# Kernel tuning notes

Measured on AMD Instinct MI355X. Metric: run time of the kernel, lower is better.

## Reference

```python
import jax, jax.numpy as jnp
import numpy as np

B, L, E = 128, 512, 128
NUM_Q, NUM_C, DIFF = 10000, 300, 100


def _lin(k, fan_in, fan_out):
    kw, kb = jax.random.split(k)
    s = 1.0 / np.sqrt(fan_in)
    W = jax.random.uniform(kw, (fan_in, fan_out), jnp.float32, -s, s)
    b = jax.random.uniform(kb, (fan_out,), jnp.float32, -s, s)
    return W, b


def setup_inputs() -> dict:
    key = jax.random.key(0)
    ks = jax.random.split(key, 24)
    inp = {
        "q": jax.random.randint(ks[0], (B, L), 0, NUM_Q),
        "c": jax.random.randint(ks[1], (B, L), 0, NUM_C),
        "sd": jax.random.randint(ks[2], (B, L), 0, DIFF + 99),
        "qd": jax.random.randint(ks[3], (B, L), 0, DIFF + 99),
        "a": jax.random.randint(ks[4], (B, L), 0, 2 * NUM_Q + 1),
        "qshft": jax.random.randint(ks[5], (B, L), 0, NUM_Q),
        "cshft": jax.random.randint(ks[6], (B, L), 0, NUM_C),
        "sdshft": jax.random.randint(ks[7], (B, L), 0, DIFF + 99),
        "qdshft": jax.random.randint(ks[8], (B, L), 0, DIFF + 99),
        "knowledge": jax.random.normal(ks[9], (1, E), jnp.float32) * 0.1,
        "q_tab": jax.random.normal(ks[10], (NUM_Q + 1, E), jnp.float32),
        "c_tab": jax.random.normal(ks[11], (NUM_C + 1, E), jnp.float32),
        "sd_tab": jax.random.normal(ks[12], (DIFF + 100, E), jnp.float32),
        "qd_tab": jax.random.normal(ks[13], (DIFF + 100, E), jnp.float32),
        "a_tab": jax.random.normal(ks[14], (2 * NUM_Q + 2, E), jnp.float32),
    }
    for name, fan_in, ki in [("1", 4 * E, 15), ("2", E, 16), ("3", E, 17),
                             ("4", 2 * E, 18), ("5", 2 * E, 19), ("6", 4 * E, 20)]:
        W, b = _lin(ks[ki], fan_in, E)
        inp[f"W{name}"], inp[f"b{name}"] = W, b
    Wf, bf = _lin(ks[21], E, 10)
    inp["Wf"], inp["bf"] = Wf, bf
    return inp


def reference(q, c, sd, qd, a, qshft, cshft, sdshft, qdshft,
              knowledge, q_tab, c_tab, sd_tab, qd_tab, a_tab,
              W1, b1, W2, b2, W3, b3, W4, b4, W5, b5, W6, b6, Wf, bf):
    # Embedding lookups  [B, L, E]
    q_e, c_e = q_tab[q], c_tab[c]
    sd_e, qd_e = sd_tab[sd], qd_tab[qd]
    a_e = a_tab[a]
    # input_data = linear_1(cat(q,c,sd,qd))  [B, L, E]
    inp = jnp.concatenate([q_e, c_e, sd_e, qd_e], -1) @ W1 + b1
    # (target_data in the torch code is dead: never used for the output)

    k0 = jnp.broadcast_to(knowledge, (q.shape[0], knowledge.shape[1]))  # [B, E]

    def step(k, xs):
        x, sd1, a1, qd1 = xs  # each [B, E]
        qq = x - k
        SDFt = jax.nn.sigmoid(qq @ W2 + b2) * jnp.tanh(qq @ W3 + b3)  # dropout=eval
        xa = jnp.concatenate([SDFt, a1], -1)
        PKAt = jax.nn.sigmoid(xa @ W4 + b4) * jnp.tanh(xa @ W5 + b5)
        ins = jnp.concatenate([k, a1, sd1, qd1], -1)
        gK = jax.nn.sigmoid(ins @ W6 + b6)
        k_new = gK * k + (1.0 - gK) * PKAt
        return k_new, k_new @ Wf + bf

    xs = (jnp.swapaxes(inp, 0, 1), jnp.swapaxes(sd_e, 0, 1),
          jnp.swapaxes(a_e, 0, 1), jnp.swapaxes(qd_e, 0, 1))  # [L, B, E]
    _, logits = jax.lax.scan(step, k0, xs)  # [L, B, 10]
    return jax.nn.sigmoid(jnp.swapaxes(logits, 0, 1))  # [B, L, 10]
```

## Files before the change

kernel.cpp:

```cpp
#include <hip/hip_runtime.h>
#include <hip/hip_bf16.h>
#include <stdint.h>

#define E_DIM 128
#define L_SEQ 512
#define B_SZ  128

typedef _Float16 h2 __attribute__((ext_vector_type(2)));
typedef _Float16 f16x8 __attribute__((ext_vector_type(8)));
typedef float f32x4 __attribute__((ext_vector_type(4)));

constexpr size_t SZ_W12 = 512 * 128 * 4;
constexpr size_t SZ_TQ  = 10001 * 128 * 4;
constexpr size_t SZ_TC  = 301 * 128 * 4;
constexpr size_t SZ_TS  = 200 * 128 * 4;
constexpr size_t SZ_TA  = 20002 * 128 * 4;

constexpr size_t OFF_W12  = 0;
constexpr size_t OFF_W13  = OFF_W12 + SZ_W12;
constexpr size_t OFF_BV2  = OFF_W13 + SZ_W12;
constexpr size_t OFF_BV3  = OFF_BV2 + 512;
constexpr size_t OFF_TQ2  = OFF_BV3 + 512;
constexpr size_t OFF_TQ3  = OFF_TQ2 + SZ_TQ;
constexpr size_t OFF_TC2  = OFF_TQ3 + SZ_TQ;
constexpr size_t OFF_TC3  = OFF_TC2 + SZ_TC;
constexpr size_t OFF_TSD2 = OFF_TC3 + SZ_TC;
constexpr size_t OFF_TSD3 = OFF_TSD2 + SZ_TS;
constexpr size_t OFF_TSD6 = OFF_TSD3 + SZ_TS;
constexpr size_t OFF_TQD2 = OFF_TSD6 + SZ_TS;
constexpr size_t OFF_TQD3 = OFF_TQD2 + SZ_TS;
constexpr size_t OFF_TQD6 = OFF_TQD3 + SZ_TS;
constexpr size_t OFF_TA4  = OFF_TQD6 + SZ_TS;
constexpr size_t OFF_TA5  = OFF_TA4 + SZ_TA;
constexpr size_t OFF_TA6  = OFF_TA5 + SZ_TA;
constexpr size_t OFF_K    = OFF_TA6 + SZ_TA;

__device__ __forceinline__ float fdot2f(unsigned int a, unsigned int b, float c) {
#if __has_builtin(__builtin_amdgcn_fdot2)
  return __builtin_amdgcn_fdot2(__builtin_bit_cast(h2, a), __builtin_bit_cast(h2, b), c, false);
#else
  h2 x = __builtin_bit_cast(h2, a), y = __builtin_bit_cast(h2, b);
  return c + (float)x[0] * (float)y[0] + (float)x[1] * (float)y[1];
#endif
}

__device__ __forceinline__ unsigned int packh2(float a, float b) {
  h2 v; v[0] = (_Float16)a; v[1] = (_Float16)b;
  return __builtin_bit_cast(unsigned int, v);
}

__device__ __forceinline__ float fsig(float x) {
  float t = __builtin_amdgcn_exp2f(-1.4426950408889634f * x);
  return __builtin_amdgcn_rcpf(1.0f + t);
}
__device__ __forceinline__ float ftanh(float x) {
  float t = __builtin_amdgcn_exp2f(2.8853900817779268f * x);
  return 1.0f - 2.0f * __builtin_amdgcn_rcpf(t + 1.0f);
}

#define BARRIER_RAW() asm volatile("s_waitcnt lgkmcnt(0)\n\ts_barrier" ::: "memory")

__global__ __launch_bounds__(128, 1) void prepA_kernel(
    const float* __restrict__ W1, const float* __restrict__ W2, const float* __restrict__ W3,
    const float* __restrict__ b1, const float* __restrict__ b2, const float* __restrict__ b3,
    char* __restrict__ ws) {
  float* W12 = (float*)(ws + OFF_W12);
  float* W13 = (float*)(ws + OFF_W13);
  float* bv2 = (float*)(ws + OFF_BV2);
  float* bv3 = (float*)(ws + OFF_BV3);
  __shared__ __align__(16) float rowb[8][128];
  const int j = threadIdx.x;
  const int blk = blockIdx.x;
  if (blk < 8) {
    const float* M = (blk < 4) ? W2 : W3;
    float* dst = (blk < 4) ? W12 : W13;
    const int r0 = (blk & 3) * 128;
    float Mcol[128];
#pragma unroll
    for (int t = 0; t < 128; t++) Mcol[t] = M[t * 128 + j];
    for (int rb = 0; rb < 128; rb += 8) {
#pragma unroll
      for (int rr = 0; rr < 8; rr++) rowb[rr][j] = W1[(r0 + rb + rr) * 128 + j];
      __syncthreads();
#pragma unroll
      for (int rr = 0; rr < 8; rr++) {
        float acc = 0.0f;
        const float4* r4 = (const float4*)rowb[rr];
#pragma unroll
        for (int t4 = 0; t4 < 32; t4++) {
          float4 v = r4[t4];
          acc += v.x * Mcol[4 * t4 + 0];
          acc += v.y * Mcol[4 * t4 + 1];
          acc += v.z * Mcol[4 * t4 + 2];
          acc += v.w * Mcol[4 * t4 + 3];
        }
        dst[(r0 + rb + rr) * 128 + j] = acc;
      }
      __syncthreads();
    }
  } else {
    rowb[0][j] = b1[j];
    __syncthreads();
    float a2 = b2[j], a3 = b3[j];
    for (int t = 0; t < 128; t++) {
      float bb = rowb[0][t];
      a2 += bb * W2[t * 128 + j];
      a3 += bb * W3[t * 128 + j];
    }
    bv2[j] = a2;
    bv3[j] = a3;
  }
}

template <int NSEG>
__global__ __launch_bounds__(256, 1) void gemm_tabs_kernel(
    const float* __restrict__ q_tab, const float* __restrict__ c_tab,
    const float* __restrict__ sd_tab, const float* __restrict__ qd_tab,
    const float* __restrict__ a_tab,
    const float* __restrict__ W4, const float* __restrict__ W5, const float* __restrict__ W6,
    const float* __restrict__ b4, const float* __restrict__ b5, const float* __restrict__ b6,
    char* __restrict__ ws) {
  constexpr int WD  = NSEG * 128;
  constexpr int SPAN = WD / 4;
  constexpr int NCT = SPAN / 16;

  __shared__ _Float16 BT[WD][136];
  __shared__ _Float16 At[32][136];
  __shared__ float biasL[384];

  const float* W12 = (const float*)(ws + OFF_W12);
  const float* W13 = (const float*)(ws + OFF_W13);
  const float* bv2 = (const float*)(ws + OFF_BV2);
  const float* bv3 = (const float*)(ws + OFF_BV3);

  const int bid = blockIdx.x;
  const int tid = threadIdx.x;
  const int wv = tid >> 6, ln = tid & 63;

  const float* src; int rows; int blk_in;
  const float* bsrc[3]; int koff[3]; const float* bias[3]; float* dst[3];
  if (NSEG == 2) {
    if (bid < 79) { src = q_tab; rows = 10001; blk_in = bid;
      bsrc[0] = W12; bsrc[1] = W13; koff[0] = koff[1] = 0;
      bias[0] = bv2; bias[1] = bv3;
      dst[0] = (float*)(ws + OFF_TQ2); dst[1] = (float*)(ws + OFF_TQ3);
    } else { src = c_tab; rows = 301; blk_in = bid - 79;
      bsrc[0] = W12; bsrc[1] = W13; koff[0] = koff[1] = 128;
      bias[0] = bias[1] = nullptr;
      dst[0] = (float*)(ws + OFF_TC2); dst[1] = (float*)(ws + OFF_TC3);
    }
    bsrc[2] = nullptr; koff[2] = 0; bias[2] = nullptr; dst[2] = nullptr;
  } else {
    if (bid < 2) { src = sd_tab; rows = 200; blk_in = bid;
      bsrc[0] = W12; bsrc[1] = W13; bsrc[2] = W6; koff[0] = koff[1] = koff[2] = 256;
      bias[0] = bias[1] = bias[2] = nullptr;
      dst[0] = (float*)(ws + OFF_TSD2); dst[1] = (float*)(ws + OFF_TSD3); dst[2] = (float*)(ws + OFF_TSD6);
    } else if (bid < 4) { src = qd_tab; rows = 200; blk_in = bid - 2;
      bsrc[0] = W12; bsrc[1] = W13; bsrc[2] = W6; koff[0] = koff[1] = koff[2] = 384;
      bias[0] = bias[1] = bias[2] = nullptr;
      dst[0] = (float*)(ws + OFF_TQD2); dst[1] = (float*)(ws + OFF_TQD3); dst[2] = (float*)(ws + OFF_TQD6);
    } else { src = a_tab; rows = 20002; blk_in = bid - 4;
      bsrc[0] = W4; bsrc[1] = W5; bsrc[2] = W6; koff[0] = koff[1] = koff[2] = 128;
      bias[0] = b4; bias[1] = b5; bias[2] = b6;
      dst[0] = (float*)(ws + OFF_TA4); dst[1] = (float*)(ws + OFF_TA5); dst[2] = (float*)(ws + OFF_TA6);
    }
  }

#pragma unroll
  for (int s = 0; s < NSEG; s++) {
    const float* M = bsrc[s] + (size_t)koff[s] * 128;
    const int jj = tid & 127, kb = tid >> 7;
    for (int k0 = 0; k0 < 128; k0 += 2) {
      const int k = k0 + kb;
      BT[s * 128 + jj][k] = (_Float16)M[k * 128 + jj];
    }
    if (tid < 128) biasL[s * 128 + tid] = bias[s] ? bias[s][tid] : 0.0f;
  }
  __syncthreads();

  f16x8 bf[NCT][4];
#pragma unroll
  for (int ct = 0; ct < NCT; ct++)
#pragma unroll
    for (int kt = 0; kt < 4; kt++) {
      const int col = wv * SPAN + ct * 16 + (ln & 15);
      const int k = kt * 32 + (ln >> 4) * 8;
      bf[ct][kt] = *(const f16x8*)&BT[col][k];
    }
  float bvl[NCT];
#pragma unroll
  for (int ct = 0; ct < NCT; ct++) bvl[ct] = biasL[wv * SPAN + ct * 16 + (ln & 15)];

  const int row_base = blk_in * 128;
  for (int ch = 0; ch < 4; ch++) {
    const int row0 = row_base + ch * 32;
    {
      const int r = tid >> 3, cb = (tid & 7) * 16;
      int sr = row0 + r; if (sr >= rows) sr = rows - 1;
      const float4* s4 = (const float4*)(src + (size_t)sr * 128 + cb);
      float4 v0 = s4[0], v1 = s4[1], v2 = s4[2], v3 = s4[3];
      f16x8 lo, hi;
      lo[0] = (_Float16)v0.x; lo[1] = (_Float16)v0.y; lo[2] = (_Float16)v0.z; lo[3] = (_Float16)v0.w;
      lo[4] = (_Float16)v1.x; lo[5] = (_Float16)v1.y; lo[6] = (_Float16)v1.z; lo[7] = (_Float16)v1.w;
      hi[0] = (_Float16)v2.x; hi[1] = (_Float16)v2.y; hi[2] = (_Float16)v2.z; hi[3] = (_Float16)v2.w;
      hi[4] = (_Float16)v3.x; hi[5] = (_Float16)v3.y; hi[6] = (_Float16)v3.z; hi[7] = (_Float16)v3.w;
      *(f16x8*)&At[r][cb] = lo;
      *(f16x8*)&At[r][cb + 8] = hi;
    }
    __syncthreads();
    f16x8 af[2][4];
#pragma unroll
    for (int rt = 0; rt < 2; rt++)
#pragma unroll
      for (int kt = 0; kt < 4; kt++) {
        const int row = rt * 16 + (ln & 15);
        const int k = kt * 32 + (ln >> 4) * 8;
        af[rt][kt] = *(const f16x8*)&At[row][k];
      }
    f32x4 acc[2][NCT];
#pragma unroll
    for (int rt = 0; rt < 2; rt++)
#pragma unroll
      for (int ct = 0; ct < NCT; ct++) acc[rt][ct] = (f32x4){0.f, 0.f, 0.f, 0.f};
#pragma unroll
    for (int kt = 0; kt < 4; kt++)
#pragma unroll
      for (int ct = 0; ct < NCT; ct++)
#pragma unroll
        for (int rt = 0; rt < 2; rt++)
          acc[rt][ct] = __builtin_amdgcn_mfma_f32_16x16x32_f16(af[rt][kt], bf[ct][kt], acc[rt][ct], 0, 0, 0);
#pragma unroll
    for (int ct = 0; ct < NCT; ct++) {
      const int gcol = wv * SPAN + ct * 16 + (ln & 15);
      const int seg = gcol >> 7, col = gcol & 127;
      float* D = dst[seg];
      const float bv = bvl[ct];
#pragma unroll
      for (int rt = 0; rt < 2; rt++)
#pragma unroll
        for (int e = 0; e < 4; e++) {
          const int row = row0 + rt * 16 + (ln >> 4) * 4 + e;
          if (row < rows) D[(size_t)row * 128 + col] = acc[rt][ct][e] + bv;
        }
    }
    __syncthreads();
  }
}


#define PREFETCH(S, P) do {                                                   \
    int _s = (S);                                                             \
    int _qi = idxb[0][_s], _ci = idxb[1][_s], _si = idxb[2][_s];              \
    int _di = idxb[3][_s], _ai = idxb[4][_s];                                 \
    P##q2 = Tq2[_qi * 128 + j]; P##q3 = Tq3[_qi * 128 + j];                   \
    P##c2 = Tc2[_ci * 128 + j]; P##c3 = Tc3[_ci * 128 + j];                   \
    P##s2 = Ts2[_si * 128 + j]; P##s3 = Ts3[_si * 128 + j];                   \
    P##s6 = Ts6[_si * 128 + j];                                               \
    P##d2 = Td2[_di * 128 + j]; P##d3 = Td3[_di * 128 + j];                   \
    P##d6 = Td6[_di * 128 + j];                                               \
    P##a4 = Ta4[_ai * 128 + j]; P##a5 = Ta5[_ai * 128 + j];                   \
    P##a6 = Ta6[_ai * 128 + j];                                               \
  } while (0)

#define SCAN_STEP(P, S2, L) do {                                              \
    float u2a = 0.f, u2b = 0.f, u3a = 0.f, u3b = 0.f, u6a = 0.f, u6b = 0.f;   \
    {                                                                         \
      const uint4* kp4 = ((const uint4*)kpair) + 8 * h;                       \
      _Pragma("unroll")                                                       \
      for (int i = 0; i < 8; i++) {                                           \
        uint4 kv = kp4[i];                                                    \
        u2a = fdot2f(kv.x, w2h[4 * i + 0], u2a);                              \
        u3a = fdot2f(kv.x, w3h[4 * i + 0], u3a);                              \
        u6a = fdot2f(kv.x, w6h[4 * i + 0], u6a);                              \
        u2b = fdot2f(kv.y, w2h[4 * i + 1], u2b);                              \
        u3b = fdot2f(kv.y, w3h[4 * i + 1], u3b);                              \
        u6b = fdot2f(kv.y, w6h[4 * i + 1], u6b);                              \
        u2a = fdot2f(kv.z, w2h[4 * i + 2], u2a);                              \
        u3a = fdot2f(kv.z, w3h[4 * i + 2], u3a);                              \
        u6a = fdot2f(kv.z, w6h[4 * i + 2], u6a);                              \
        u2b = fdot2f(kv.w, w2h[4 * i + 3], u2b);                              \
        u3b = fdot2f(kv.w, w3h[4 * i + 3], u3b);                              \
        u6b = fdot2f(kv.w, w6h[4 * i + 3], u6b);                              \
      }                                                                       \
    }                                                                         \
    float U2p = u2a + u2b, U3p = u3a + u3b, U6p = u6a + u6b;                  \
    U2p += __shfl_xor(U2p, 32);                                               \
    U3p += __shfl_xor(U3p, 32);                                               \
    U6p += __shfl_xor(U6p, 32);                                               \
    float U2 = (P##q2 + P##c2 + P##s2 + P##d2) - U2p;                         \
    float U3 = (P##q3 + P##c3 + P##s3 + P##d3) - U3p;                         \
    float U6 = (P##a6 + P##s6 + P##d6) + U6p;                                 \
    float sdft = fsig(U2) * ftanh(U3);                                        \
    float g = fsig(U6);                                                       \
    if (!h) ((_Float16*)sdfp)[j] = (_Float16)sdft;                            \
    BARRIER_RAW();                                    \
    float u4a = 0.f, u4b = 0.f, u5a = 0.f, u5b = 0.f;                         \
    {                                                                         \
      const uint4* sp4 = ((const uint4*)sdfp) + 8 * h;                        \
      _Pragma("unroll")                                                       \
      for (int i = 0; i < 8; i++) {                                           \
        uint4 sv = sp4[i];                                                    \
        u4a = fdot2f(sv.x, w4h[4 * i + 0], u4a);                              \
        u5a = fdot2f(sv.x, w5h[4 * i + 0], u5a);                              \
        u4b = fdot2f(sv.y, w4h[4 * i + 1], u4b);                              \
        u5b = fdot2f(sv.y, w5h[4 * i + 1], u5b);                              \
        u4a = fdot2f(sv.z, w4h[4 * i + 2], u4a);                              \
        u5a = fdot2f(sv.z, w5h[4 * i + 2], u5a);                              \
        u4b = fdot2f(sv.w, w4h[4 * i + 3], u4b);                              \
        u5b = fdot2f(sv.w, w5h[4 * i + 3], u5b);                              \
      }                                                                       \
    }                                                                         \
    float U4p = u4a + u4b, U5p = u5a + u5b;                                   \
    U4p += __shfl_xor(U4p, 32);                                               \
    U5p += __shfl_xor(U5p, 32);                                               \
    float pk = fsig(U4p + P##a4) * ftanh(U5p + P##a5);                        \
    k = g * k + (1.0f - g) * pk;                                              \
    if (h) ((_Float16*)kpair)[j] = (_Float16)k;                               \
    if (!h) Kout[((size_t)(base + (L))) * 128 + j] = k;                       \
    PREFETCH(S2, P);                                                          \
    BARRIER_RAW();                                       \
  } while (0)

__global__ __launch_bounds__(256, 1) void scan_kernel(
    const int* __restrict__ q, const int* __restrict__ c, const int* __restrict__ sd,
    const int* __restrict__ qd, const int* __restrict__ a,
    const float* __restrict__ knowledge,
    const float* __restrict__ W2, const float* __restrict__ W3, const float* __restrict__ W4,
    const float* __restrict__ W5, const float* __restrict__ W6,
    char* __restrict__ ws) {
  const int tid = threadIdx.x;
  const int wv = tid >> 6, ln = tid & 63;
  const int j = (wv << 5) | (ln & 31);
  const int h = ln >> 5;
  const int b = blockIdx.x;
  const int base = b * L_SEQ;

  const float* Tq2 = (const float*)(ws + OFF_TQ2);
  const float* Tq3 = (const float*)(ws + OFF_TQ3);
  const float* Tc2 = (const float*)(ws + OFF_TC2);
  const float* Tc3 = (const float*)(ws + OFF_TC3);
  const float* Ts2 = (const float*)(ws + OFF_TSD2);
  const float* Ts3 = (const float*)(ws + OFF_TSD3);
  const float* Ts6 = (const float*)(ws + OFF_TSD6);
  const float* Td2 = (const float*)(ws + OFF_TQD2);
  const float* Td3 = (const float*)(ws + OFF_TQD3);
  const float* Td6 = (const float*)(ws + OFF_TQD6);
  const float* Ta4 = (const float*)(ws + OFF_TA4);
  const float* Ta5 = (const float*)(ws + OFF_TA5);
  const float* Ta6 = (const float*)(ws + OFF_TA6);
  float* Kout = (float*)(ws + OFF_K);

  __shared__ int idxb[5][L_SEQ];
  __shared__ __align__(16) unsigned int kpair[64];
  __shared__ __align__(16) unsigned int sdfp[64];

  idxb[0][tid] = q[base + tid];  idxb[0][tid + 256] = q[base + tid + 256];
  idxb[1][tid] = c[base + tid];  idxb[1][tid + 256] = c[base + tid + 256];
  idxb[2][tid] = sd[base + tid]; idxb[2][tid + 256] = sd[base + tid + 256];
  idxb[3][tid] = qd[base + tid]; idxb[3][tid + 256] = qd[base + tid + 256];
  idxb[4][tid] = a[base + tid];  idxb[4][tid + 256] = a[base + tid + 256];

  unsigned int w2h[32], w3h[32], w6h[32], w4h[32], w5h[32];
  const int t0 = h * 64;
#pragma unroll
  for (int p = 0; p < 32; p++) {
    w2h[p] = packh2(W2[(t0 + 2 * p) * 128 + j], W2[(t0 + 2 * p + 1) * 128 + j]);
    w3h[p] = packh2(W3[(t0 + 2 * p) * 128 + j], W3[(t0 + 2 * p + 1) * 128 + j]);
    w6h[p] = packh2(W6[(t0 + 2 * p) * 128 + j], W6[(t0 + 2 * p + 1) * 128 + j]);
    w4h[p] = packh2(W4[(t0 + 2 * p) * 128 + j], W4[(t0 + 2 * p + 1) * 128 + j]);
    w5h[p] = packh2(W5[(t0 + 2 * p) * 128 + j], W5[(t0 + 2 * p + 1) * 128 + j]);
  }

  float k = knowledge[j];
  if (h) ((_Float16*)kpair)[j] = (_Float16)k;
  __syncthreads();

  float gAq2, gAq3, gAc2, gAc3, gAs2, gAs3, gAs6, gAd2, gAd3, gAd6, gAa4, gAa5, gAa6;
  float gBq2, gBq3, gBc2, gBc3, gBs2, gBs3, gBs6, gBd2, gBd3, gBd6, gBa4, gBa5, gBa6;
  PREFETCH(0, gA);
  PREFETCH(1, gB);

#pragma unroll 1
  for (int m = 0; m < L_SEQ / 2; m++) {
    const int l0 = 2 * m;
    const int s2 = (l0 + 2 < L_SEQ) ? (l0 + 2) : (L_SEQ - 1);
    const int s3 = (l0 + 3 < L_SEQ) ? (l0 + 3) : (L_SEQ - 1);
    SCAN_STEP(gA, s2, l0);
    SCAN_STEP(gB, s3, l0 + 1);
  }
}

__global__ __launch_bounds__(256, 2) void logits_kernel(
    const float* __restrict__ Wf, const float* __restrict__ bf,
    const char* __restrict__ ws, float* __restrict__ out) {
  __shared__ float WfL[1280];
  __shared__ float bfL[10];
  const int tid = threadIdx.x;
  for (int i = tid; i < 1280; i += 256) WfL[i] = Wf[i];
  if (tid < 10) bfL[tid] = bf[tid];
  __syncthreads();
  const float* K = (const float*)(ws + OFF_K);
  const int nrows = B_SZ * L_SEQ;
  for (int r = blockIdx.x * 256 + tid; r < nrows; r += gridDim.x * 256) {
    const float4* kr = (const float4*)(K + (size_t)r * 128);
    float acc[10];
#pragma unroll
    for (int i = 0; i < 10; i++) acc[i] = bfL[i];
#pragma unroll
    for (int t4 = 0; t4 < 32; t4++) {
      float4 v = kr[t4];
#pragma unroll
      for (int i = 0; i < 10; i++)
        acc[i] += v.x * WfL[(4 * t4 + 0) * 10 + i] + v.y * WfL[(4 * t4 + 1) * 10 + i] +
                  v.z * WfL[(4 * t4 + 2) * 10 + i] + v.w * WfL[(4 * t4 + 3) * 10 + i];
    }
    float* o = out + (size_t)r * 10;
#pragma unroll
    for (int i = 0; i < 10; i++) o[i] = fsig(acc[i]);
  }
}

extern "C" void kernel_launch(void* const* d_in, const int* in_sizes, int n_in,
                              void* d_out, int out_size, void* d_ws, size_t ws_size,
                              hipStream_t stream) {
  const int* q  = (const int*)d_in[0];
  const int* c  = (const int*)d_in[1];
  const int* sd = (const int*)d_in[2];
  const int* qd = (const int*)d_in[3];
  const int* a  = (const int*)d_in[4];
  const float* knowledge = (const float*)d_in[9];
  const float* q_tab  = (const float*)d_in[10];
  const float* c_tab  = (const float*)d_in[11];
  const float* sd_tab = (const float*)d_in[12];
  const float* qd_tab = (const float*)d_in[13];
  const float* a_tab  = (const float*)d_in[14];
  const float* W1 = (const float*)d_in[15];
  const float* b1 = (const float*)d_in[16];
  const float* W2 = (const float*)d_in[17];
  const float* b2 = (const float*)d_in[18];
  const float* W3 = (const float*)d_in[19];
  const float* b3 = (const float*)d_in[20];
  const float* W4 = (const float*)d_in[21];
  const float* b4 = (const float*)d_in[22];
  const float* W5 = (const float*)d_in[23];
  const float* b5 = (const float*)d_in[24];
  const float* W6 = (const float*)d_in[25];
  const float* b6 = (const float*)d_in[26];
  const float* Wf = (const float*)d_in[27];
  const float* bf = (const float*)d_in[28];
  char* ws = (char*)d_ws;
  float* out = (float*)d_out;

  prepA_kernel<<<9, 128, 0, stream>>>(W1, W2, W3, b1, b2, b3, ws);
  gemm_tabs_kernel<2><<<82, 256, 0, stream>>>(q_tab, c_tab, sd_tab, qd_tab, a_tab,
                                              W4, W5, W6, b4, b5, b6, ws);
  gemm_tabs_kernel<3><<<161, 256, 0, stream>>>(q_tab, c_tab, sd_tab, qd_tab, a_tab,
                                               W4, W5, W6, b4, b5, b6, ws);
  scan_kernel<<<B_SZ, 256, 0, stream>>>(q, c, sd, qd, a, knowledge, W2, W3, W4, W5, W6, ws);
  logits_kernel<<<256, 256, 0, stream>>>(Wf, bf, ws, out);
}
```

Before: 793.8 us.

## Repartition precompute kernels across more blocks and pack two sequences per scan block

The W1·W2/W1·W3 fold is spread over 513 small blocks instead of 9, and the two table-GEMM launches become one launch with 647 blocks, one output matrix each. This is meant to raise GPU occupancy in the preparation phase. The scan kernel now runs two independent batch sequences per 512-thread block, each with its own index and shared exchange buffers. That halves the scan grid to 64 blocks but lets the two sequences' barrier-bound latency overlap on a CU, at the cost of block-wide barriers coupling the two groups.

After: 883.6 us. 1.11x slower.

```diff
diff --git a/kernel.cpp b/kernel.cpp
--- a/kernel.cpp
+++ b/kernel.cpp
@@ -60,7 +60,7 @@
 
 #define BARRIER_RAW() asm volatile("s_waitcnt lgkmcnt(0)\n\ts_barrier" ::: "memory")
 
-__global__ __launch_bounds__(128, 1) void prepA_kernel(
+__global__ __launch_bounds__(256, 2) void prepA_kernel(
     const float* __restrict__ W1, const float* __restrict__ W2, const float* __restrict__ W3,
     const float* __restrict__ b1, const float* __restrict__ b2, const float* __restrict__ b3,
     char* __restrict__ ws) {
@@ -68,130 +68,110 @@
   float* W13 = (float*)(ws + OFF_W13);
   float* bv2 = (float*)(ws + OFF_BV2);
   float* bv3 = (float*)(ws + OFF_BV3);
-  __shared__ __align__(16) float rowb[8][128];
-  const int j = threadIdx.x;
-  const int blk = blockIdx.x;
-  if (blk < 8) {
-    const float* M = (blk < 4) ? W2 : W3;
-    float* dst = (blk < 4) ? W12 : W13;
-    const int r0 = (blk & 3) * 128;
-    float Mcol[128];
-#pragma unroll
-    for (int t = 0; t < 128; t++) Mcol[t] = M[t * 128 + j];
-    for (int rb = 0; rb < 128; rb += 8) {
-#pragma unroll
-      for (int rr = 0; rr < 8; rr++) rowb[rr][j] = W1[(r0 + rb + rr) * 128 + j];
-      __syncthreads();
-#pragma unroll
-      for (int rr = 0; rr < 8; rr++) {
-        float acc = 0.0f;
-        const float4* r4 = (const float4*)rowb[rr];
-#pragma unroll
-        for (int t4 = 0; t4 < 32; t4++) {
-          float4 v = r4[t4];
-          acc += v.x * Mcol[4 * t4 + 0];
-          acc += v.y * Mcol[4 * t4 + 1];
-          acc += v.z * Mcol[4 * t4 + 2];
-          acc += v.w * Mcol[4 * t4 + 3];
-        }
-        dst[(r0 + rb + rr) * 128 + j] = acc;
-      }
-      __syncthreads();
+  const int blk = blockIdx.x, tid = threadIdx.x;
+  if (blk < 512) {
+    const int m = blk >> 8;
+    const int rp = blk & 255;
+    const float* M = m ? W3 : W2;
+    float* dst = m ? W13 : W12;
+    const int rr = tid >> 7, j = tid & 127;
+    const int r = rp * 2 + rr;
+    __shared__ float rowL[2][128];
+    rowL[rr][j] = W1[r * 128 + j];
+    __syncthreads();
+    float acc = 0.0f;
+#pragma unroll 8
+    for (int t = 0; t < 128; t++) acc += rowL[rr][t] * M[t * 128 + j];
+    dst[r * 128 + j] = acc;
+  } else if (tid < 128) {
+    float a2 = b2[tid], a3 = b3[tid];
+    for (int t = 0; t < 128; t++) {
+      float bb = b1[t];
+      a2 += bb * W2[t * 128 + tid];
+      a3 += bb * W3[t * 128 + tid];
     }
-  } else {
-    rowb[0][j] = b1[j];
-    __syncthreads();
-    float a2 = b2[j], a3 = b3[j];
-    for (int t = 0; t < 128; t++) {
-      float bb = rowb[0][t];
-      a2 += bb * W2[t * 128 + j];
-      a3 += bb * W3[t * 128 + j];
-    }
-    bv2[j] = a2;
-    bv3[j] = a3;
-  }
-}
-
-template <int NSEG>
-__global__ __launch_bounds__(256, 1) void gemm_tabs_kernel(
+    bv2[tid] = a2;
+    bv3[tid] = a3;
+  }
+}
+
+__global__ __launch_bounds__(256, 2) void gemm_tab1_kernel(
     const float* __restrict__ q_tab, const float* __restrict__ c_tab,
     const float* __restrict__ sd_tab, const float* __restrict__ qd_tab,
     const float* __restrict__ a_tab,
     const float* __restrict__ W4, const float* __restrict__ W5, const float* __restrict__ W6,
     const float* __restrict__ b4, const float* __restrict__ b5, const float* __restrict__ b6,
     char* __restrict__ ws) {
-  constexpr int WD  = NSEG * 128;
-  constexpr int SPAN = WD / 4;
-  constexpr int NCT = SPAN / 16;
-
-  __shared__ _Float16 BT[WD][136];
+  __shared__ _Float16 BT[128][136];
   __shared__ _Float16 At[32][136];
-  __shared__ float biasL[384];
+  __shared__ float biasL[128];
 
   const float* W12 = (const float*)(ws + OFF_W12);
   const float* W13 = (const float*)(ws + OFF_W13);
-  const float* bv2 = (const float*)(ws + OFF_BV2);
-  const float* bv3 = (const float*)(ws + OFF_BV3);
-
-  const int bid = blockIdx.x;
-  const int tid = threadIdx.x;
+  const float* bv2f = (const float*)(ws + OFF_BV2);
+  const float* bv3f = (const float*)(ws + OFF_BV3);
+
+  const int bid = blockIdx.x, tid = threadIdx.x;
   const int wv = tid >> 6, ln = tid & 63;
 
-  const float* src; int rows; int blk_in;
-  const float* bsrc[3]; int koff[3]; const float* bias[3]; float* dst[3];
-  if (NSEG == 2) {
-    if (bid < 79) { src = q_tab; rows = 10001; blk_in = bid;
-      bsrc[0] = W12; bsrc[1] = W13; koff[0] = koff[1] = 0;
-      bias[0] = bv2; bias[1] = bv3;
-      dst[0] = (float*)(ws + OFF_TQ2); dst[1] = (float*)(ws + OFF_TQ3);
-    } else { src = c_tab; rows = 301; blk_in = bid - 79;
-      bsrc[0] = W12; bsrc[1] = W13; koff[0] = koff[1] = 128;
-      bias[0] = bias[1] = nullptr;
-      dst[0] = (float*)(ws + OFF_TC2); dst[1] = (float*)(ws + OFF_TC3);
+  int task, rb;
+  if      (bid < 79)  { task = 0;  rb = bid; }
+  else if (bid < 158) { task = 1;  rb = bid - 79; }
+  else if (bid < 161) { task = 2;  rb = bid - 158; }
+  else if (bid < 164) { task = 3;  rb = bid - 161; }
+  else if (bid < 166) { task = 4;  rb = bid - 164; }
+  else if (bid < 168) { task = 5;  rb = bid - 166; }
+  else if (bid < 170) { task = 6;  rb = bid - 168; }
+  else if (bid < 172) { task = 7;  rb = bid - 170; }
+  else if (bid < 174) { task = 8;  rb = bid - 172; }
+  else if (bid < 176) { task = 9;  rb = bid - 174; }
+  else if (bid < 333) { task = 10; rb = bid - 176; }
+  else if (bid < 490) { task = 11; rb = bid - 333; }
+  else                { task = 12; rb = bid - 490; }
+
+  const float* src; int rows; const float* Bsrc; const float* bias; float* dst;
+  switch (task) {
+    case 0:  src = q_tab;  rows = 10001; Bsrc = W12;            bias = bv2f;   dst = (float*)(ws + OFF_TQ2);  break;
+    case 1:  src = q_tab;  rows = 10001; Bsrc = W13;            bias = bv3f;   dst = (float*)(ws + OFF_TQ3);  break;
+    case 2:  src = c_tab;  rows = 301;   Bsrc = W12 + 128*128;  bias = nullptr; dst = (float*)(ws + OFF_TC2);  break;
+    case 3:  src = c_tab;  rows = 301;   Bsrc = W13 + 128*128;  bias = nullptr; dst = (float*)(ws + OFF_TC3);  break;
+    case 4:  src = sd_tab; rows = 200;   Bsrc = W12 + 256*128;  bias = nullptr; dst = (float*)(ws + OFF_TSD2); break;
+    case 5:  src = sd_tab; rows = 200;   Bsrc = W13 + 256*128;  bias = nullptr; dst = (float*)(ws + OFF_TSD3); break;
+    case 6:  src = sd_tab; rows = 200;   Bsrc = W6  + 256*128;  bias = nullptr; dst = (float*)(ws + OFF_TSD6); break;
+    case 7:  src = qd_tab; rows = 200;   Bsrc = W12 + 384*128;  bias = nullptr; dst = (float*)(ws + OFF_TQD2); break;
+    case 8:  src = qd_tab; rows = 200;   Bsrc = W13 + 384*128;  bias = nullptr; dst = (float*)(ws + OFF_TQD3); break;
+    case 9:  src = qd_tab; rows = 200;   Bsrc = W6  + 384*128;  bias = nullptr; dst = (float*)(ws + OFF_TQD6); break;
+    case 10: src = a_tab;  rows = 20002; Bsrc = W4  + 128*128;  bias = b4;     dst = (float*)(ws + OFF_TA4);  break;
+    case 11: src = a_tab;  rows = 20002; Bsrc = W5  + 128*128;  bias = b5;     dst = (float*)(ws + OFF_TA5);  break;
+    default: src = a_tab;  rows = 20002; Bsrc = W6  + 128*128;  bias = b6;     dst = (float*)(ws + OFF_TA6);  break;
+  }
+
+#pragma unroll
+  for (int r = 0; r < 8; r++) {
+    const int k = (tid >> 4) + r * 16;
+    const int j0 = (tid & 15) * 8;
+    float4 v0 = *(const float4*)(Bsrc + k * 128 + j0);
+    float4 v1 = *(const float4*)(Bsrc + k * 128 + j0 + 4);
+    BT[j0 + 0][k] = (_Float16)v0.x; BT[j0 + 1][k] = (_Float16)v0.y;
+    BT[j0 + 2][k] = (_Float16)v0.z; BT[j0 + 3][k] = (_Float16)v0.w;
+    BT[j0 + 4][k] = (_Float16)v1.x; BT[j0 + 5][k] = (_Float16)v1.y;
+    BT[j0 + 6][k] = (_Float16)v1.z; BT[j0 + 7][k] = (_Float16)v1.w;
+  }
+  if (tid < 128) biasL[tid] = bias ? bias[tid] : 0.0f;
+  __syncthreads();
+
+  f16x8 bfr[2][4];
+#pragma unroll
+  for (int ct = 0; ct < 2; ct++)
+#pragma unroll
+    for (int kt = 0; kt < 4; kt++) {
+      const int col = wv * 32 + ct * 16 + (ln & 15);
+      const int k = kt * 32 + (ln >> 4) * 8;
+      bfr[ct][kt] = *(const f16x8*)&BT[col][k];
     }
-    bsrc[2] = nullptr; koff[2] = 0; bias[2] = nullptr; dst[2] = nullptr;
-  } else {
-    if (bid < 2) { src = sd_tab; rows = 200; blk_in = bid;
-      bsrc[0] = W12; bsrc[1] = W13; bsrc[2] = W6; koff[0] = koff[1] = koff[2] = 256;
-      bias[0] = bias[1] = bias[2] = nullptr;
-      dst[0] = (float*)(ws + OFF_TSD2); dst[1] = (float*)(ws + OFF_TSD3); dst[2] = (float*)(ws + OFF_TSD6);
-    } else if (bid < 4) { src = qd_tab; rows = 200; blk_in = bid - 2;
-      bsrc[0] = W12; bsrc[1] = W13; bsrc[2] = W6; koff[0] = koff[1] = koff[2] = 384;
-      bias[0] = bias[1] = bias[2] = nullptr;
-      dst[0] = (float*)(ws + OFF_TQD2); dst[1] = (float*)(ws + OFF_TQD3); dst[2] = (float*)(ws + OFF_TQD6);
-    } else { src = a_tab; rows = 20002; blk_in = bid - 4;
-      bsrc[0] = W4; bsrc[1] = W5; bsrc[2] = W6; koff[0] = koff[1] = koff[2] = 128;
-      bias[0] = b4; bias[1] = b5; bias[2] = b6;
-      dst[0] = (float*)(ws + OFF_TA4); dst[1] = (float*)(ws + OFF_TA5); dst[2] = (float*)(ws + OFF_TA6);
-    }
-  }
-
-#pragma unroll
-  for (int s = 0; s < NSEG; s++) {
-    const float* M = bsrc[s] + (size_t)koff[s] * 128;
-    const int jj = tid & 127, kb = tid >> 7;
-    for (int k0 = 0; k0 < 128; k0 += 2) {
-      const int k = k0 + kb;
-      BT[s * 128 + jj][k] = (_Float16)M[k * 128 + jj];
-    }
-    if (tid < 128) biasL[s * 128 + tid] = bias[s] ? bias[s][tid] : 0.0f;
-  }
-  __syncthreads();
-
-  f16x8 bf[NCT][4];
-#pragma unroll
-  for (int ct = 0; ct < NCT; ct++)
-#pragma unroll
-    for (int kt = 0; kt < 4; kt++) {
-      const int col = wv * SPAN + ct * 16 + (ln & 15);
-      const int k = kt * 32 + (ln >> 4) * 8;
-      bf[ct][kt] = *(const f16x8*)&BT[col][k];
-    }
-  float bvl[NCT];
-#pragma unroll
-  for (int ct = 0; ct < NCT; ct++) bvl[ct] = biasL[wv * SPAN + ct * 16 + (ln & 15)];
-
-  const int row_base = blk_in * 128;
+  float bvl[2] = { biasL[wv * 32 + (ln & 15)], biasL[wv * 32 + 16 + (ln & 15)] };
+
+  const int row_base = rb * 128;
   for (int ch = 0; ch < 4; ch++) {
     const int row0 = row_base + ch * 32;
     {
@@ -217,30 +197,28 @@
         const int k = kt * 32 + (ln >> 4) * 8;
         af[rt][kt] = *(const f16x8*)&At[row][k];
       }
-    f32x4 acc[2][NCT];
+    f32x4 acc[2][2];
 #pragma unroll
     for (int rt = 0; rt < 2; rt++)
 #pragma unroll
-      for (int ct = 0; ct < NCT; ct++) acc[rt][ct] = (f32x4){0.f, 0.f, 0.f, 0.f};
+      for (int ct = 0; ct < 2; ct++) acc[rt][ct] = (f32x4){0.f, 0.f, 0.f, 0.f};
 #pragma unroll
     for (int kt = 0; kt < 4; kt++)
 #pragma unroll
-      for (int ct = 0; ct < NCT; ct++)
+      for (int ct = 0; ct < 2; ct++)
 #pragma unroll
         for (int rt = 0; rt < 2; rt++)
-          acc[rt][ct] = __builtin_amdgcn_mfma_f32_16x16x32_f16(af[rt][kt], bf[ct][kt], acc[rt][ct], 0, 0, 0);
-#pragma unroll
-    for (int ct = 0; ct < NCT; ct++) {
-      const int gcol = wv * SPAN + ct * 16 + (ln & 15);
-      const int seg = gcol >> 7, col = gcol & 127;
-      float* D = dst[seg];
+          acc[rt][ct] = __builtin_amdgcn_mfma_f32_16x16x32_f16(af[rt][kt], bfr[ct][kt], acc[rt][ct], 0, 0, 0);
+#pragma unroll
+    for (int ct = 0; ct < 2; ct++) {
+      const int col = wv * 32 + ct * 16 + (ln & 15);
       const float bv = bvl[ct];
 #pragma unroll
       for (int rt = 0; rt < 2; rt++)
 #pragma unroll
         for (int e = 0; e < 4; e++) {
           const int row = row0 + rt * 16 + (ln >> 4) * 4 + e;
-          if (row < rows) D[(size_t)row * 128 + col] = acc[rt][ct][e] + bv;
+          if (row < rows) dst[(size_t)row * 128 + col] = acc[rt][ct][e] + bv;
         }
     }
     __syncthreads();
@@ -250,8 +228,8 @@
 
 #define PREFETCH(S, P) do {                                                   \
     int _s = (S);                                                             \
-    int _qi = idxb[0][_s], _ci = idxb[1][_s], _si = idxb[2][_s];              \
-    int _di = idxb[3][_s], _ai = idxb[4][_s];                                 \
+    int _qi = idxb[g][0][_s], _ci = idxb[g][1][_s], _si = idxb[g][2][_s];     \
+    int _di = idxb[g][3][_s], _ai = idxb[g][4][_s];                           \
     P##q2 = Tq2[_qi * 128 + j]; P##q3 = Tq3[_qi * 128 + j];                   \
     P##c2 = Tc2[_ci * 128 + j]; P##c3 = Tc3[_ci * 128 + j];                   \
     P##s2 = Ts2[_si * 128 + j]; P##s3 = Ts3[_si * 128 + j];                   \
@@ -265,7 +243,7 @@
 #define SCAN_STEP(P, S2, L) do {                                              \
     float u2a = 0.f, u2b = 0.f, u3a = 0.f, u3b = 0.f, u6a = 0.f, u6b = 0.f;   \
     {                                                                         \
-      const uint4* kp4 = ((const uint4*)kpair) + 8 * h;                       \
+      const uint4* kp4 = ((const uint4*)kpair[g]) + 8 * h;                    \
       _Pragma("unroll")                                                       \
       for (int i = 0; i < 8; i++) {                                           \
         uint4 kv = kp4[i];                                                    \
@@ -291,12 +269,12 @@
     float U3 = (P##q3 + P##c3 + P##s3 + P##d3) - U3p;                         \
     float U6 = (P##a6 + P##s6 + P##d6) + U6p;                                 \
     float sdft = fsig(U2) * ftanh(U3);                                        \
-    float g = fsig(U6);                                                       \
-    if (!h) ((_Float16*)sdfp)[j] = (_Float16)sdft;                            \
+    float g_ = fsig(U6);                                                      \
+    if (!h) ((_Float16*)sdfp[g])[j] = (_Float16)sdft;                         \
     BARRIER_RAW();                                    \
     float u4a = 0.f, u4b = 0.f, u5a = 0.f, u5b = 0.f;                         \
     {                                                                         \
-      const uint4* sp4 = ((const uint4*)sdfp) + 8 * h;                        \
+      const uint4* sp4 = ((const uint4*)sdfp[g]) + 8 * h;                     \
       _Pragma("unroll")                                                       \
       for (int i = 0; i < 8; i++) {                                           \
         uint4 sv = sp4[i];                                                    \
@@ -314,14 +292,14 @@
     U4p += __shfl_xor(U4p, 32);                                               \
     U5p += __shfl_xor(U5p, 32);                                               \
     float pk = fsig(U4p + P##a4) * ftanh(U5p + P##a5);                        \
-    k = g * k + (1.0f - g) * pk;                                              \
-    if (h) ((_Float16*)kpair)[j] = (_Float16)k;                               \
+    k = g_ * k + (1.0f - g_) * pk;                                            \
+    if (h) ((_Float16*)kpair[g])[j] = (_Float16)k;                            \
     if (!h) Kout[((size_t)(base + (L))) * 128 + j] = k;                       \
     PREFETCH(S2, P);                                                          \
     BARRIER_RAW();                                       \
   } while (0)
 
-__global__ __launch_bounds__(256, 1) void scan_kernel(
+__global__ __launch_bounds__(512, 2) void scan_kernel(
     const int* __restrict__ q, const int* __restrict__ c, const int* __restrict__ sd,
     const int* __restrict__ qd, const int* __restrict__ a,
     const float* __restrict__ knowledge,
@@ -329,10 +307,13 @@
     const float* __restrict__ W5, const float* __restrict__ W6,
     char* __restrict__ ws) {
   const int tid = threadIdx.x;
-  const int wv = tid >> 6, ln = tid & 63;
-  const int j = (wv << 5) | (ln & 31);
+  const int g = tid >> 8;
+  const int t256 = tid & 255;
+  const int ln = tid & 63;
+  const int wvl = (t256 >> 6);
+  const int j = (wvl << 5) | (ln & 31);
   const int h = ln >> 5;
-  const int b = blockIdx.x;
+  const int b = (blockIdx.x << 1) | g;
   const int base = b * L_SEQ;
 
   const float* Tq2 = (const float*)(ws + OFF_TQ2);
@@ -350,15 +331,15 @@
   const float* Ta6 = (const float*)(ws + OFF_TA6);
   float* Kout = (float*)(ws + OFF_K);
 
-  __shared__ int idxb[5][L_SEQ];
-  __shared__ __align__(16) unsigned int kpair[64];
-  __shared__ __align__(16) unsigned int sdfp[64];
-
-  idxb[0][tid] = q[base + tid];  idxb[0][tid + 256] = q[base + tid + 256];
-  idxb[1][tid] = c[base + tid];  idxb[1][tid + 256] = c[base + tid + 256];
-  idxb[2][tid] = sd[base + tid]; idxb[2][tid + 256] = sd[base + tid + 256];
-  idxb[3][tid] = qd[base + tid]; idxb[3][tid + 256] = qd[base + tid + 256];
-  idxb[4][tid] = a[base + tid];  idxb[4][tid + 256] = a[base + tid + 256];
+  __shared__ int idxb[2][5][L_SEQ];
+  __shared__ __align__(16) unsigned int kpair[2][64];
+  __shared__ __align__(16) unsigned int sdfp[2][64];
+
+  idxb[g][0][t256] = q[base + t256];  idxb[g][0][t256 + 256] = q[base + t256 + 256];
+  idxb[g][1][t256] = c[base + t256];  idxb[g][1][t256 + 256] = c[base + t256 + 256];
+  idxb[g][2][t256] = sd[base + t256]; idxb[g][2][t256 + 256] = sd[base + t256 + 256];
+  idxb[g][3][t256] = qd[base + t256]; idxb[g][3][t256 + 256] = qd[base + t256 + 256];
+  idxb[g][4][t256] = a[base + t256];  idxb[g][4][t256 + 256] = a[base + t256 + 256];
 
   unsigned int w2h[32], w3h[32], w6h[32], w4h[32], w5h[32];
   const int t0 = h * 64;
@@ -372,7 +353,7 @@
   }
 
   float k = knowledge[j];
-  if (h) ((_Float16*)kpair)[j] = (_Float16)k;
+  if (h) ((_Float16*)kpair[g])[j] = (_Float16)k;
   __syncthreads();
 
   float gAq2, gAq3, gAc2, gAc3, gAs2, gAs3, gAs6, gAd2, gAd3, gAd6, gAa4, gAa5, gAa6;
@@ -451,11 +432,9 @@
   char* ws = (char*)d_ws;
   float* out = (float*)d_out;
 
-  prepA_kernel<<<9, 128, 0, stream>>>(W1, W2, W3, b1, b2, b3, ws);
-  gemm_tabs_kernel<2><<<82, 256, 0, stream>>>(q_tab, c_tab, sd_tab, qd_tab, a_tab,
-                                              W4, W5, W6, b4, b5, b6, ws);
-  gemm_tabs_kernel<3><<<161, 256, 0, stream>>>(q_tab, c_tab, sd_tab, qd_tab, a_tab,
-                                               W4, W5, W6, b4, b5, b6, ws);
-  scan_kernel<<<B_SZ, 256, 0, stream>>>(q, c, sd, qd, a, knowledge, W2, W3, W4, W5, W6, ws);
+  prepA_kernel<<<513, 256, 0, stream>>>(W1, W2, W3, b1, b2, b3, ws);
+  gemm_tab1_kernel<<<647, 256, 0, stream>>>(q_tab, c_tab, sd_tab, qd_tab, a_tab,
+                                            W4, W5, W6, b4, b5, b6, ws);
+  scan_kernel<<<B_SZ / 2, 512, 0, stream>>>(q, c, sd, qd, a, knowledge, W2, W3, W4, W5, W6, ws);
   logits_kernel<<<256, 256, 0, stream>>>(Wf, bf, ws, out);
 }
```
